# Kernel optimization log

Hardware: AMD Instinct MI355X
Metric: run time of the kernel (lower is better)

The kernel has to match this reference:

```python
import jax, jax.numpy as jnp
import numpy as np

N = 8192
F_IN = 256
F_OUT = 256


def setup_inputs() -> dict:
    key = jax.random.key(0)
    k1, k2, k3 = jax.random.split(key, 3)
    H = jax.random.normal(k1, (N, F_IN), dtype=jnp.float32)
    A_tilde = jax.random.uniform(k2, (N, N), dtype=jnp.float32)  # positive -> valid degrees
    # xavier_uniform for W: limit = sqrt(6/(fan_in+fan_out))
    limit = np.sqrt(6.0 / (F_IN + F_OUT)).astype(np.float32)
    W = jax.random.uniform(k3, (F_IN, F_OUT), dtype=jnp.float32, minval=-limit, maxval=limit)
    return {"H": H, "A_tilde": A_tilde, "W": W}


def reference(H, A_tilde, W):
    # H(l+1) = relu(D^-1/2 A D^-1/2 H W)
    # Diagonal matmuls expressed as row/col rescaling (same math, O(N^2)).
    d_inv_sqrt = jnp.sum(A_tilde, axis=1) ** -0.5          # [N]
    A_norm = d_inv_sqrt[:, None] * A_tilde * d_inv_sqrt[None, :]  # [N,N]
    H_next = (A_norm @ H) @ W                              # [N,F_out]
    return jax.nn.relu(H_next)
```

## Files before the change

kernel.cpp:

```cpp
#include <hip/hip_runtime.h>
#include <hip/hip_bf16.h>

#define N_ROWS 8192
#define F_DIM  256

typedef __bf16 bf16x8_t __attribute__((ext_vector_type(8)));
typedef float  f32x4_t  __attribute__((ext_vector_type(4)));

static __device__ __forceinline__ unsigned short f2bf(float x) {
    union { __hip_bfloat16 h; unsigned short u; } c;
    c.h = __float2bfloat16(x);
    return c.u;
}
static __device__ __forceinline__ unsigned pk2(float lo, float hi) {
    return (unsigned)f2bf(lo) | ((unsigned)f2bf(hi) << 16);
}

__global__ __launch_bounds__(256) void wconv_kernel(const float* __restrict__ W,
                                                    unsigned short* __restrict__ Ws) {
    const int kb = blockIdx.x;
    const int t  = threadIdx.x;
    __shared__ float wt[32][257];
    const int r = t >> 3, g = t & 7;
    const float* src = W + (kb * 32 + r) * F_DIM + g * 32;
#pragma unroll
    for (int i = 0; i < 8; ++i) {
        float4 v = *(const float4*)(src + i * 4);
        wt[r][g * 32 + i * 4 + 0] = v.x;
        wt[r][g * 32 + i * 4 + 1] = v.y;
        wt[r][g * 32 + i * 4 + 2] = v.z;
        wt[r][g * 32 + i * 4 + 3] = v.w;
    }
    __syncthreads();
    unsigned o[16];
#pragma unroll
    for (int k = 0; k < 32; k += 2) o[k >> 1] = pk2(wt[k][t], wt[k + 1][t]);
    uint4* dst = (uint4*)(Ws + kb * 8192 + t * 32);
#pragma unroll
    for (int i = 0; i < 4; ++i) dst[i] = make_uint4(o[4*i], o[4*i+1], o[4*i+2], o[4*i+3]);
}

__global__ __launch_bounds__(1024) void prep_kernel(const float* __restrict__ A,
                                                    const float* __restrict__ H,
                                                    float* __restrict__ dvec,
                                                    unsigned short* __restrict__ Xs) {
    const int kb = blockIdx.x;
    const int t  = threadIdx.x;
    __shared__ float psum[32][33];
    __shared__ float dl[32];
    __shared__ float ht[32][257];

    const int r = t >> 5, g = t & 31;
    const float* arow = A + (size_t)(kb * 32 + r) * N_ROWS;
    float s0 = 0.f, s1 = 0.f, s2 = 0.f, s3 = 0.f;
#pragma unroll 8
    for (int i = 0; i < 64; ++i) {
        float4 v = *(const float4*)(arow + (i * 32 + g) * 4);
        s0 += v.x; s1 += v.y; s2 += v.z; s3 += v.w;
    }
    psum[r][g] = (s0 + s1) + (s2 + s3);
    __syncthreads();
    if (t < 32) {
        float s = 0.f;
#pragma unroll
        for (int i = 0; i < 32; ++i) s += psum[t][i];
        float d = 1.0f / sqrtf(s);
        dl[t] = d;
        dvec[kb * 32 + t] = d;
    }
    __syncthreads();
    {
        const int hr = t >> 5, hg = t & 31;
        const float* hsrc = H + (size_t)(kb * 32 + hr) * F_DIM + hg * 8;
        float4 v0 = ((const float4*)hsrc)[0];
        float4 v1 = ((const float4*)hsrc)[1];
        const float d = dl[hr];
        ht[hr][hg * 8 + 0] = v0.x * d;
        ht[hr][hg * 8 + 1] = v0.y * d;
        ht[hr][hg * 8 + 2] = v0.z * d;
        ht[hr][hg * 8 + 3] = v0.w * d;
        ht[hr][hg * 8 + 4] = v1.x * d;
        ht[hr][hg * 8 + 5] = v1.y * d;
        ht[hr][hg * 8 + 6] = v1.z * d;
        ht[hr][hg * 8 + 7] = v1.w * d;
    }
    __syncthreads();
    const int n = t >> 2, q = t & 3;
    unsigned o[4];
#pragma unroll
    for (int i = 0; i < 4; ++i) {
        int k = q * 8 + i * 2;
        o[i] = pk2(ht[k][n], ht[k + 1][n]);
    }
    *(uint4*)(Xs + kb * 8192 + n * 32 + q * 8) = make_uint4(o[0], o[1], o[2], o[3]);
}

template <int KITERS, int ASTRIDE, bool DSCALE, bool RELU>
__global__ __launch_bounds__(512) void gemm_kernel(const float* __restrict__ Amat,
                                                   const unsigned short* __restrict__ Bs,
                                                   const float* __restrict__ dvec,
                                                   float* __restrict__ out) {
    const int t   = threadIdx.x;
    const int blk = blockIdx.x;
    const int w = t >> 6, l = t & 63;
    const int m = l & 15, q = l >> 4;

    __shared__ __align__(16) unsigned short Al[2][1024];

    const int ar = t >> 4, ac = (t & 15) * 2;
    const float* aptr = Amat + (size_t)(blk * 32 + ar) * ASTRIDE + ac;
    const int wr_idx = (ac >> 3) * 256 + (ar >> 4) * 128 + (ar & 15) * 8 + (ac & 7);

    const unsigned short* bptr = Bs + (w * 32 + m) * 32 + q * 8;

    f32x4_t acc[2][2] = {};

    float2 a_cur[2]; uint4 b_cur[2][2];
#pragma unroll
    for (int s = 0; s < 2; ++s) {
        a_cur[s]    = *(const float2*)(aptr + s * 32);
        b_cur[s][0] = *(const uint4*)(bptr + s * 8192);
        b_cur[s][1] = *(const uint4*)(bptr + s * 8192 + 512);
    }

    for (int i = 0; i < KITERS; ++i) {
        float2 a_nxt[2]; uint4 b_nxt[2][2];
        if (i + 1 < KITERS) {
            const float* ap = aptr + (i + 1) * 64;
            const unsigned short* bp = bptr + (size_t)(i + 1) * 16384;
#pragma unroll
            for (int s = 0; s < 2; ++s) {
                a_nxt[s]    = *(const float2*)(ap + s * 32);
                b_nxt[s][0] = *(const uint4*)(bp + s * 8192);
                b_nxt[s][1] = *(const uint4*)(bp + s * 8192 + 512);
            }
        }
        const unsigned aw0 = pk2(a_cur[0].x, a_cur[0].y);
        const unsigned aw1 = pk2(a_cur[1].x, a_cur[1].y);
        __syncthreads();
        *(unsigned*)&Al[0][wr_idx] = aw0;
        *(unsigned*)&Al[1][wr_idx] = aw1;
        __syncthreads();
#pragma unroll
        for (int s = 0; s < 2; ++s) {
            bf16x8_t af0 = *(const bf16x8_t*)&Al[s][q * 256 + m * 8];
            bf16x8_t af1 = *(const bf16x8_t*)&Al[s][q * 256 + 128 + m * 8];
            bf16x8_t bf0 = __builtin_bit_cast(bf16x8_t, b_cur[s][0]);
            bf16x8_t bf1 = __builtin_bit_cast(bf16x8_t, b_cur[s][1]);
            acc[0][0] = __builtin_amdgcn_mfma_f32_16x16x32_bf16(af0, bf0, acc[0][0], 0, 0, 0);
            acc[0][1] = __builtin_amdgcn_mfma_f32_16x16x32_bf16(af0, bf1, acc[0][1], 0, 0, 0);
            acc[1][0] = __builtin_amdgcn_mfma_f32_16x16x32_bf16(af1, bf0, acc[1][0], 0, 0, 0);
            acc[1][1] = __builtin_amdgcn_mfma_f32_16x16x32_bf16(af1, bf1, acc[1][1], 0, 0, 0);
        }
#pragma unroll
        for (int s = 0; s < 2; ++s) {
            a_cur[s]    = a_nxt[s];
            b_cur[s][0] = b_nxt[s][0];
            b_cur[s][1] = b_nxt[s][1];
        }
    }

    const int gcol0 = w * 32 + m;
#pragma unroll
    for (int mt = 0; mt < 2; ++mt) {
#pragma unroll
        for (int r = 0; r < 4; ++r) {
            const int grow = blk * 32 + mt * 16 + q * 4 + r;
            float ds = 1.0f;
            if (DSCALE) ds = dvec[grow];
#pragma unroll
            for (int nt = 0; nt < 2; ++nt) {
                float v = acc[mt][nt][r] * ds;
                if (RELU) v = fmaxf(v, 0.f);
                out[(size_t)grow * F_DIM + gcol0 + nt * 16] = v;
            }
        }
    }
}

extern "C" void kernel_launch(void* const* d_in, const int* in_sizes, int n_in,
                              void* d_out, int out_size, void* d_ws, size_t ws_size,
                              hipStream_t stream) {
    (void)in_sizes; (void)n_in; (void)out_size; (void)ws_size;
    const float* H = (const float*)d_in[0];
    const float* A = (const float*)d_in[1];
    const float* W = (const float*)d_in[2];
    float* out = (float*)d_out;

    char* ws = (char*)d_ws;
    float*          dvec = (float*)ws;
    unsigned short* Xs   = (unsigned short*)(ws + (32 << 10));
    unsigned short* Wsz  = (unsigned short*)(ws + (32 << 10) + (4 << 20));
    float*          Y    = (float*)(ws + (32 << 10) + (4 << 20) + (128 << 10));

    wconv_kernel<<<dim3(8),   dim3(256),  0, stream>>>(W, Wsz);
    prep_kernel <<<dim3(256), dim3(1024), 0, stream>>>(A, H, dvec, Xs);
    gemm_kernel<128, 8192, true,  false><<<dim3(256), dim3(512), 0, stream>>>(A, Xs, dvec, Y);
    gemm_kernel<4,   256,  false, true ><<<dim3(256), dim3(512), 0, stream>>>(Y, Wsz, nullptr, out);
}
```

Baseline: 464.7 us.

## Pre-convert A to bf16 and use large-tile split-K GEMM with direct LDS loads

The row-sum pass now also writes A as bf16 into workspace. The main A·X product is replaced by a 128x128-tile, split-K=2 MFMA kernel that streams bf16 tiles into double-buffered LDS via global_load_lds. The second GEMM sums the two partial results and applies the row scaling before multiplying by W. This is meant to fix the low data reuse and per-iteration conversion of the old small-tile GEMM. In exchange it adds a 128MB bf16 write and needs a large workspace.

```diff
diff --git a/kernel.cpp b/kernel.cpp
--- a/kernel.cpp
+++ b/kernel.cpp
@@ -14,6 +14,11 @@
 }
 static __device__ __forceinline__ unsigned pk2(float lo, float hi) {
     return (unsigned)f2bf(lo) | ((unsigned)f2bf(hi) << 16);
+}
+
+static __device__ __forceinline__ void gload16(const unsigned short* g, unsigned short* s) {
+    __builtin_amdgcn_global_load_lds((const __attribute__((address_space(1))) void*)g,
+                                     (__attribute__((address_space(3))) void*)s, 16, 0, 0);
 }
 
 __global__ __launch_bounds__(256) void wconv_kernel(const float* __restrict__ W,
@@ -40,10 +45,11 @@
     for (int i = 0; i < 4; ++i) dst[i] = make_uint4(o[4*i], o[4*i+1], o[4*i+2], o[4*i+3]);
 }
 
-__global__ __launch_bounds__(1024) void prep_kernel(const float* __restrict__ A,
-                                                    const float* __restrict__ H,
-                                                    float* __restrict__ dvec,
-                                                    unsigned short* __restrict__ Xs) {
+__global__ __launch_bounds__(1024) void sumconv_kernel(const float* __restrict__ A,
+                                                       const float* __restrict__ H,
+                                                       float* __restrict__ dvec,
+                                                       unsigned short* __restrict__ Abf,
+                                                       unsigned short* __restrict__ Xh) {
     const int kb = blockIdx.x;
     const int t  = threadIdx.x;
     __shared__ float psum[32][33];
@@ -51,12 +57,17 @@
     __shared__ float ht[32][257];
 
     const int r = t >> 5, g = t & 31;
-    const float* arow = A + (size_t)(kb * 32 + r) * N_ROWS;
+    const int row = kb * 32 + r;
+    const float* arow = A + (size_t)row * N_ROWS;
+    unsigned short* aout = Abf + (size_t)row * N_ROWS;
     float s0 = 0.f, s1 = 0.f, s2 = 0.f, s3 = 0.f;
 #pragma unroll 8
     for (int i = 0; i < 64; ++i) {
-        float4 v = *(const float4*)(arow + (i * 32 + g) * 4);
+        const int e = (i * 32 + g) * 4;
+        float4 v = *(const float4*)(arow + e);
         s0 += v.x; s1 += v.y; s2 += v.z; s3 += v.w;
+        uint2 p = make_uint2(pk2(v.x, v.y), pk2(v.z, v.w));
+        *(uint2*)(aout + e) = p;
     }
     psum[r][g] = (s0 + s1) + (s2 + s3);
     __syncthreads();
@@ -92,14 +103,93 @@
         int k = q * 8 + i * 2;
         o[i] = pk2(ht[k][n], ht[k + 1][n]);
     }
-    *(uint4*)(Xs + kb * 8192 + n * 32 + q * 8) = make_uint4(o[0], o[1], o[2], o[3]);
-}
-
-template <int KITERS, int ASTRIDE, bool DSCALE, bool RELU>
-__global__ __launch_bounds__(512) void gemm_kernel(const float* __restrict__ Amat,
-                                                   const unsigned short* __restrict__ Bs,
-                                                   const float* __restrict__ dvec,
-                                                   float* __restrict__ out) {
+    *(uint4*)(Xh + kb * 8192 + n * 32 + q * 8) = make_uint4(o[0], o[1], o[2], o[3]);
+}
+
+__global__ __launch_bounds__(256) void biggemm_kernel(const unsigned short* __restrict__ Abf,
+                                                      const unsigned short* __restrict__ Xh,
+                                                      float* __restrict__ Ybase) {
+    const int t = threadIdx.x;
+    const int w = t >> 6, l = t & 63;
+    const int bid = blockIdx.x;
+    const int mi = bid >> 2, ks = (bid >> 1) & 1, ni = bid & 1;
+    const int kbase = ks * 4096;
+
+    __shared__ __align__(16) unsigned short lds[2][16384];
+
+    const int m16 = l & 15, q8 = (l >> 4) * 8;
+
+    const unsigned short* ag[4];
+    const unsigned short* bg[4];
+    int aslot[4], bslot[4];
+#pragma unroll
+    for (int j = 0; j < 4; ++j) {
+        const int idx = w * 4 + j;
+        const int ft = idx >> 1, s = idx & 1;
+        ag[j] = Abf + (size_t)(mi * 128 + ft * 16 + m16) * N_ROWS + kbase + s * 32 + q8;
+        aslot[j] = idx * 512;
+        bg[j] = Xh + (size_t)((kbase >> 5) + s) * 8192
+                   + (ni * 128 + ft * 16 + m16) * 32 + q8;
+        bslot[j] = 8192 + idx * 512;
+    }
+
+    f32x4_t acc[4][4] = {};
+
+#pragma unroll
+    for (int j = 0; j < 4; ++j) {
+        gload16(ag[j], &lds[0][aslot[j]]);
+        gload16(bg[j], &lds[0][bslot[j]]);
+    }
+
+    const int wm = w & 1, wn = w >> 1;
+    const int KITERS = 64;
+    for (int i = 0; i < KITERS; ++i) {
+        __syncthreads();
+        const int cb = i & 1;
+        if (i + 1 < KITERS) {
+            const int nb = cb ^ 1;
+#pragma unroll
+            for (int j = 0; j < 4; ++j) {
+                gload16(ag[j] + (i + 1) * 64,                 &lds[nb][aslot[j]]);
+                gload16(bg[j] + (size_t)(i + 1) * 16384,      &lds[nb][bslot[j]]);
+            }
+        }
+#pragma unroll
+        for (int s = 0; s < 2; ++s) {
+            bf16x8_t af[4], bf[4];
+#pragma unroll
+            for (int x = 0; x < 4; ++x) {
+                af[x] = *(const bf16x8_t*)&lds[cb][((wm * 4 + x) * 2 + s) * 512 + l * 8];
+                bf[x] = *(const bf16x8_t*)&lds[cb][8192 + ((wn * 4 + x) * 2 + s) * 512 + l * 8];
+            }
+#pragma unroll
+            for (int x = 0; x < 4; ++x)
+#pragma unroll
+                for (int y = 0; y < 4; ++y)
+                    acc[x][y] = __builtin_amdgcn_mfma_f32_16x16x32_bf16(af[x], bf[y], acc[x][y], 0, 0, 0);
+        }
+    }
+
+    float* Y = Ybase + (size_t)ks * (N_ROWS * F_DIM);
+#pragma unroll
+    for (int x = 0; x < 4; ++x) {
+#pragma unroll
+        for (int r = 0; r < 4; ++r) {
+            const int row = mi * 128 + wm * 64 + x * 16 + (l >> 4) * 4 + r;
+#pragma unroll
+            for (int y = 0; y < 4; ++y) {
+                const int col = ni * 128 + wn * 64 + y * 16 + m16;
+                Y[(size_t)row * F_DIM + col] = acc[x][y][r];
+            }
+        }
+    }
+}
+
+__global__ __launch_bounds__(512) void outgemm_kernel(const float* __restrict__ Y0,
+                                                      const float* __restrict__ Y1,
+                                                      const unsigned short* __restrict__ Ws,
+                                                      const float* __restrict__ dvec,
+                                                      float* __restrict__ out) {
     const int t   = threadIdx.x;
     const int blk = blockIdx.x;
     const int w = t >> 6, l = t & 63;
@@ -108,29 +198,38 @@
     __shared__ __align__(16) unsigned short Al[2][1024];
 
     const int ar = t >> 4, ac = (t & 15) * 2;
-    const float* aptr = Amat + (size_t)(blk * 32 + ar) * ASTRIDE + ac;
+    const int arow = blk * 32 + ar;
+    const float* y0p = Y0 + (size_t)arow * F_DIM + ac;
+    const float* y1p = Y1 + (size_t)arow * F_DIM + ac;
+    const float ds = dvec[arow];
     const int wr_idx = (ac >> 3) * 256 + (ar >> 4) * 128 + (ar & 15) * 8 + (ac & 7);
 
-    const unsigned short* bptr = Bs + (w * 32 + m) * 32 + q * 8;
+    const unsigned short* bptr = Ws + (w * 32 + m) * 32 + q * 8;
 
     f32x4_t acc[2][2] = {};
 
     float2 a_cur[2]; uint4 b_cur[2][2];
 #pragma unroll
     for (int s = 0; s < 2; ++s) {
-        a_cur[s]    = *(const float2*)(aptr + s * 32);
+        float2 u0 = *(const float2*)(y0p + s * 32);
+        float2 u1 = *(const float2*)(y1p + s * 32);
+        a_cur[s] = make_float2((u0.x + u1.x) * ds, (u0.y + u1.y) * ds);
         b_cur[s][0] = *(const uint4*)(bptr + s * 8192);
         b_cur[s][1] = *(const uint4*)(bptr + s * 8192 + 512);
     }
 
+    const int KITERS = 4;
     for (int i = 0; i < KITERS; ++i) {
         float2 a_nxt[2]; uint4 b_nxt[2][2];
         if (i + 1 < KITERS) {
-            const float* ap = aptr + (i + 1) * 64;
+            const float* p0 = y0p + (i + 1) * 64;
+            const float* p1 = y1p + (i + 1) * 64;
             const unsigned short* bp = bptr + (size_t)(i + 1) * 16384;
 #pragma unroll
             for (int s = 0; s < 2; ++s) {
-                a_nxt[s]    = *(const float2*)(ap + s * 32);
+                float2 u0 = *(const float2*)(p0 + s * 32);
+                float2 u1 = *(const float2*)(p1 + s * 32);
+                a_nxt[s] = make_float2((u0.x + u1.x) * ds, (u0.y + u1.y) * ds);
                 b_nxt[s][0] = *(const uint4*)(bp + s * 8192);
                 b_nxt[s][1] = *(const uint4*)(bp + s * 8192 + 512);
             }
@@ -154,7 +253,7 @@
         }
 #pragma unroll
         for (int s = 0; s < 2; ++s) {
-            a_cur[s]    = a_nxt[s];
+            a_cur[s] = a_nxt[s];
             b_cur[s][0] = b_nxt[s][0];
             b_cur[s][1] = b_nxt[s][1];
         }
@@ -166,12 +265,10 @@
 #pragma unroll
         for (int r = 0; r < 4; ++r) {
             const int grow = blk * 32 + mt * 16 + q * 4 + r;
-            float ds = 1.0f;
-            if (DSCALE) ds = dvec[grow];
 #pragma unroll
             for (int nt = 0; nt < 2; ++nt) {
-                float v = acc[mt][nt][r] * ds;
-                if (RELU) v = fmaxf(v, 0.f);
+                float v = acc[mt][nt][r];
+                v = fmaxf(v, 0.f);
                 out[(size_t)grow * F_DIM + gcol0 + nt * 16] = v;
             }
         }
@@ -188,13 +285,18 @@
     float* out = (float*)d_out;
 
     char* ws = (char*)d_ws;
-    float*          dvec = (float*)ws;
-    unsigned short* Xs   = (unsigned short*)(ws + (32 << 10));
-    unsigned short* Wsz  = (unsigned short*)(ws + (32 << 10) + (4 << 20));
-    float*          Y    = (float*)(ws + (32 << 10) + (4 << 20) + (128 << 10));
-
-    wconv_kernel<<<dim3(8),   dim3(256),  0, stream>>>(W, Wsz);
-    prep_kernel <<<dim3(256), dim3(1024), 0, stream>>>(A, H, dvec, Xs);
-    gemm_kernel<128, 8192, true,  false><<<dim3(256), dim3(512), 0, stream>>>(A, Xs, dvec, Y);
-    gemm_kernel<4,   256,  false, true ><<<dim3(256), dim3(512), 0, stream>>>(Y, Wsz, nullptr, out);
-}
+    size_t off = 0;
+    float*          dvec = (float*)(ws + off);           off += (32 << 10);
+    unsigned short* Xh   = (unsigned short*)(ws + off);  off += (4 << 20);
+    unsigned short* Wsz  = (unsigned short*)(ws + off);  off += (128 << 10);
+    float*          Y    = (float*)(ws + off);           off += (16 << 20);
+    unsigned short* Abf  = (unsigned short*)(ws + off);  off += (size_t)N_ROWS * N_ROWS * 2;
+
+    float* Y0 = Y;
+    float* Y1 = Y + (size_t)N_ROWS * F_DIM;
+
+    wconv_kernel  <<<dim3(8),   dim3(256),  0, stream>>>(W, Wsz);
+    sumconv_kernel<<<dim3(256), dim3(1024), 0, stream>>>(A, H, dvec, Abf, Xh);
+    biggemm_kernel<<<dim3(256), dim3(256),  0, stream>>>(Abf, Xh, Y);
+    outgemm_kernel<<<dim3(256), dim3(512),  0, stream>>>(Y0, Y1, Wsz, dvec, out);
+}
```

New measurement: 518.2 us. +11.5%, slower.
